# Kernel optimization log

Measured on AMD Instinct MI355X. Metric: run time of the kernel, lower is better.

## Reference

```python
import jax, jax.numpy as jnp
import numpy as np
import math

B, C, H, W = 8, 256, 64, 64
CQK = C // 8

def _conv1x1(x, w, b):
    # x: [B,C,H,W], w: [O,C], b: [O]  (1x1 conv == per-pixel linear)
    return jnp.einsum('bchw,oc->bohw', x, w) + b[None, :, None, None]

def setup_inputs() -> dict:
    key = jax.random.key(0)
    ks = jax.random.split(key, 7)
    inputs = jax.random.normal(ks[0], (B, C, H, W), dtype=jnp.float32)
    # init_weight: normal(0, sqrt(2/(k*k*out_channels))) for 1x1 convs
    wq = jax.random.normal(ks[1], (CQK, C), dtype=jnp.float32) * math.sqrt(2.0 / CQK)
    wk = jax.random.normal(ks[2], (CQK, C), dtype=jnp.float32) * math.sqrt(2.0 / CQK)
    wv = jax.random.normal(ks[3], (C, C), dtype=jnp.float32) * math.sqrt(2.0 / C)
    bq = jnp.zeros((CQK,), dtype=jnp.float32)
    bk = jnp.zeros((CQK,), dtype=jnp.float32)
    bv = jnp.zeros((C,), dtype=jnp.float32)
    # torch init is zeros(1); use nonzero so the attention path contributes
    alpha = jnp.full((1,), 0.5, dtype=jnp.float32)
    return {"inputs": inputs, "wq": wq, "bq": bq, "wk": wk, "bk": bk,
            "wv": wv, "bv": bv, "alpha": alpha}

def reference(inputs, wq, bq, wk, bk, wv, bv, alpha):
    b, c, h, w = inputs.shape
    n = h * w
    q = _conv1x1(inputs, wq, bq).reshape(b, -1, n)          # [B, C/8, N]
    k = _conv1x1(inputs, wk, bk).reshape(b, -1, n)          # [B, C/8, N]
    v = _conv1x1(inputs, wv, bv).reshape(b, c, n)           # [B, C, N]
    # attention_weight[b, i, j] = q[:, i] . k[:, j]
    attn = jnp.einsum('bdi,bdj->bij', q, k)                 # [B, N, N]
    attn = jax.nn.softmax(attn, axis=-1)
    # value @ attn^T : out[b, c, i] = sum_j v[b, c, j] * attn[b, i, j]
    out = jnp.einsum('bcj,bij->bci', v, attn)               # [B, C, N]
    return alpha[0] * out.reshape(inputs.shape) + inputs
```

## Files before the change

### kernel.cpp

```cpp
#include <hip/hip_runtime.h>
#include <math.h>

#define B_  8
#define C_  256
#define N_  4096
#define NJC (N_ / 128)
#define PLD 136

using frag  = __attribute__((ext_vector_type(8))) short;
using f32x4 = __attribute__((ext_vector_type(4))) float;

__device__ __forceinline__ unsigned short f2bf(float f) {
    unsigned u = __float_as_uint(f);
    u += 0x7fffu + ((u >> 16) & 1u);
    return (unsigned short)(u >> 16);
}
__device__ __forceinline__ float bf2f(unsigned short h) {
    return __uint_as_float(((unsigned)h) << 16);
}
#define PK2(a, b) (((unsigned)(a)) | (((unsigned)(b)) << 16))

__device__ __forceinline__ f32x4 fmax4(f32x4 a, f32x4 b) {
    f32x4 r;
    r[0] = fmaxf(a[0], b[0]); r[1] = fmaxf(a[1], b[1]);
    r[2] = fmaxf(a[2], b[2]); r[3] = fmaxf(a[3], b[3]);
    return r;
}

__global__ __launch_bounds__(256) void wprep_kernel(
    const float* __restrict__ wq, const float* __restrict__ wk,
    const float* __restrict__ wv,
    unsigned short* __restrict__ whf, unsigned short* __restrict__ wlf)
{
    const int fid  = blockIdx.x * 256 + threadIdx.x;
    if (fid >= 20 * 8 * 64) return;
    const int g    = fid >> 9;
    const int kc   = (fid >> 6) & 7;
    const int lane = fid & 63;
    const int r16  = lane & 15, q = lane >> 4;

    const float* src; int row;
    if (g < 2)      { src = wq; row = g * 16 + r16; }
    else if (g < 4) { src = wk; row = (g - 2) * 16 + r16; }
    else            { src = wv; row = (g - 4) * 16 + r16; }

    const float* wp = src + row * 256 + kc * 32 + q * 8;
    float v[8];
#pragma unroll
    for (int j = 0; j < 8; ++j) v[j] = wp[j];

    unsigned short h[8];
#pragma unroll
    for (int j = 0; j < 8; ++j) h[j] = f2bf(v[j]);
    uint4 U;
    U.x = PK2(h[0], h[1]); U.y = PK2(h[2], h[3]);
    U.z = PK2(h[4], h[5]); U.w = PK2(h[6], h[7]);
    *(uint4*)&whf[(size_t)fid * 8] = U;

    if (g < 4) {
        unsigned short l[8];
#pragma unroll
        for (int j = 0; j < 8; ++j) l[j] = f2bf(v[j] - bf2f(h[j]));
        uint4 V;
        V.x = PK2(l[0], l[1]); V.y = PK2(l[2], l[3]);
        V.z = PK2(l[4], l[5]); V.w = PK2(l[6], l[7]);
        *(uint4*)&wlf[(size_t)fid * 8] = V;
    }
}

__global__ __launch_bounds__(256, 2) void proj_kernel(
    const float* __restrict__ x,
    const float* __restrict__ bq, const float* __restrict__ bk,
    const float* __restrict__ bv,
    const unsigned short* __restrict__ whf, const unsigned short* __restrict__ wlf,
    unsigned short* __restrict__ qh, unsigned short* __restrict__ ql,
    unsigned short* __restrict__ kh, unsigned short* __restrict__ kl,
    unsigned short* __restrict__ vbf)
{
    __shared__ unsigned xpk[64 * 260 + 4];

    const int tid  = threadIdx.x;
    const int w    = tid >> 6;
    const int lane = tid & 63;
    const int quad = lane >> 4;
    const int l16  = lane & 15;
    const int n0   = blockIdx.x * 64;
    const int b    = blockIdx.y;

    {
        const int p  = tid & 63;
        const int cb = tid >> 6;
        const float* xbase = x + (size_t)b * C_ * N_ + n0 + p;
#pragma unroll 16
        for (int s = 0; s < 64; ++s) {
            const int c = s * 4 + cb;
            const float v = xbase[(size_t)c * N_];
            const unsigned short hb = f2bf(v);
            const unsigned short lb = f2bf(v - bf2f(hb));
            xpk[p * 260 + c] = (((unsigned)hb) << 16) | lb;
        }
    }
    __syncthreads();

    const frag* wh = (const frag*)whf;
    const frag* wl = (const frag*)wlf;
    const int n = n0 + w * 16 + l16;

    f32x4 acc[20];
#pragma unroll
    for (int g = 0; g < 20; ++g) acc[g] = (f32x4){0.f, 0.f, 0.f, 0.f};

    for (int kc = 0; kc < 8; ++kc) {
        const unsigned* row = &xpk[(w * 16 + l16) * 260 + kc * 32 + quad * 8];
        const uint4 A  = *(const uint4*)row;
        const uint4 Bv = *(const uint4*)(row + 4);
        frag bh, bl;
        unsigned* bhp = (unsigned*)&bh;
        unsigned* blp = (unsigned*)&bl;
        bhp[0] = __builtin_amdgcn_perm(A.y,  A.x,  0x07060302u);
        bhp[1] = __builtin_amdgcn_perm(A.w,  A.z,  0x07060302u);
        bhp[2] = __builtin_amdgcn_perm(Bv.y, Bv.x, 0x07060302u);
        bhp[3] = __builtin_amdgcn_perm(Bv.w, Bv.z, 0x07060302u);
        blp[0] = __builtin_amdgcn_perm(A.y,  A.x,  0x05040100u);
        blp[1] = __builtin_amdgcn_perm(A.w,  A.z,  0x05040100u);
        blp[2] = __builtin_amdgcn_perm(Bv.y, Bv.x, 0x05040100u);
        blp[3] = __builtin_amdgcn_perm(Bv.w, Bv.z, 0x05040100u);

#pragma unroll
        for (int g = 0; g < 4; ++g) {
            const frag ah = wh[(g * 8 + kc) * 64 + lane];
            const frag al = wl[(g * 8 + kc) * 64 + lane];
            acc[g] = __builtin_amdgcn_mfma_f32_16x16x32_bf16(ah, bh, acc[g], 0, 0, 0);
            acc[g] = __builtin_amdgcn_mfma_f32_16x16x32_bf16(al, bh, acc[g], 0, 0, 0);
            acc[g] = __builtin_amdgcn_mfma_f32_16x16x32_bf16(ah, bl, acc[g], 0, 0, 0);
        }
#pragma unroll
        for (int g = 4; g < 20; ++g) {
            const frag ah = wh[(g * 8 + kc) * 64 + lane];
            acc[g] = __builtin_amdgcn_mfma_f32_16x16x32_bf16(ah, bh, acc[g], 0, 0, 0);
        }
    }

#pragma unroll
    for (int g = 0; g < 4; ++g) {
        const bool isq = (g < 2);
        const float* bias = isq ? bq : bk;
        const int dbase = (isq ? g : g - 2) * 16 + quad * 4;
        unsigned short hs[4], ls[4];
#pragma unroll
        for (int r = 0; r < 4; ++r) {
            const float f = acc[g][r] + bias[dbase + r];
            hs[r] = f2bf(f);
            ls[r] = f2bf(f - bf2f(hs[r]));
        }
        const size_t off = ((size_t)(b * N_ + n)) * 32 + dbase;
        *(uint2*)&(isq ? qh : kh)[off] = make_uint2(PK2(hs[0], hs[1]), PK2(hs[2], hs[3]));
        *(uint2*)&(isq ? ql : kl)[off] = make_uint2(PK2(ls[0], ls[1]), PK2(ls[2], ls[3]));
    }
#pragma unroll
    for (int g = 4; g < 20; ++g) {
#pragma unroll
        for (int r = 0; r < 4; ++r) {
            const int c = (g - 4) * 16 + quad * 4 + r;
            vbf[((size_t)b * C_ + c) * N_ + n] = f2bf(acc[g][r] + bv[c]);
        }
    }
}

__global__ __launch_bounds__(512, 2) void attn_kernel(
    const unsigned short* __restrict__ qh, const unsigned short* __restrict__ ql,
    const unsigned short* __restrict__ khg, const unsigned short* __restrict__ klg,
    const unsigned short* __restrict__ vbf,
    const float* __restrict__ x, const float* __restrict__ alpha_p,
    float* __restrict__ out)
{
    __shared__ __align__(16) short kbuf[2][2][128 * 32];
    __shared__ __align__(16) short p_s[2][128 * PLD];
    __shared__ float alpha_s[2][128];
    __shared__ float l_s[128];

    const int tid  = threadIdx.x;
    const int w    = tid >> 6;
    const int lane = tid & 63;
    const int quad = lane >> 4;
    const int l16  = lane & 15;
    const int b    = blockIdx.y;
    const int i0   = blockIdx.x * 128;

    const size_t qoff = ((size_t)(b * N_ + i0 + w * 16 + l16)) * 32 + quad * 8;
    const frag qhf = *(const frag*)(qh + qoff);
    const frag qlf = *(const frag*)(ql + qoff);

    const unsigned short* khb = khg + (size_t)b * N_ * 32;
    const unsigned short* klb = klg + (size_t)b * N_ * 32;
    const unsigned short* vb  = vbf + (size_t)b * C_ * N_;

    f32x4 o[8][2];
#pragma unroll
    for (int it = 0; it < 8; ++it) {
        o[it][0] = (f32x4){0.f, 0.f, 0.f, 0.f};
        o[it][1] = (f32x4){0.f, 0.f, 0.f, 0.f};
    }

    float m_run = -INFINITY, l_run = 0.f;

    const int stoff = w * 512 + lane * 8;

    {
        const uint4 h0 = *(const uint4*)(khb + stoff);
        const uint4 l0 = *(const uint4*)(klb + stoff);
        *(uint4*)&kbuf[0][0][stoff] = h0;
        *(uint4*)&kbuf[0][1][stoff] = l0;
    }
    __syncthreads();

    for (int jc = 0; jc < NJC; ++jc) {
        const int bf = jc & 1;

        f32x4 st[8];
#pragma unroll
        for (int js = 0; js < 8; ++js) {
            const frag ka = *(const frag*)&kbuf[bf][0][(js * 16 + l16) * 32 + quad * 8];
            const frag kb2 = *(const frag*)&kbuf[bf][1][(js * 16 + l16) * 32 + quad * 8];
            f32x4 s = (f32x4){0.f, 0.f, 0.f, 0.f};
            s = __builtin_amdgcn_mfma_f32_16x16x32_bf16(ka, qhf, s, 0, 0, 0);
            s = __builtin_amdgcn_mfma_f32_16x16x32_bf16(ka, qlf, s, 0, 0, 0);
            s = __builtin_amdgcn_mfma_f32_16x16x32_bf16(kb2, qhf, s, 0, 0, 0);
            st[js] = s;
        }

        const int jn = (jc + 1 < NJC) ? jc + 1 : jc;
        const uint4 knh = *(const uint4*)(khb + (size_t)jn * 4096 + stoff);
        const uint4 knl = *(const uint4*)(klb + (size_t)jn * 4096 + stoff);

        f32x4 t0 = fmax4(fmax4(st[0], st[1]), fmax4(st[2], st[3]));
        f32x4 t1 = fmax4(fmax4(st[4], st[5]), fmax4(st[6], st[7]));
        t0 = fmax4(t0, t1);
        float mx = fmaxf(fmaxf(t0[0], t0[1]), fmaxf(t0[2], t0[3]));
        mx = fmaxf(mx, __shfl_xor(mx, 16));
        mx = fmaxf(mx, __shfl_xor(mx, 32));
        const float mnew = fmaxf(m_run, mx);
        const float sc   = __expf(m_run - mnew);

        f32x4 ps4 = (f32x4){0.f, 0.f, 0.f, 0.f};
#pragma unroll
        for (int js = 0; js < 8; ++js) {
#pragma unroll
            for (int r = 0; r < 4; ++r) st[js][r] = __expf(st[js][r] - mnew);
            ps4[0] += st[js][0]; ps4[1] += st[js][1];
            ps4[2] += st[js][2]; ps4[3] += st[js][3];
        }
        float ps = (ps4[0] + ps4[1]) + (ps4[2] + ps4[3]);
        ps += __shfl_xor(ps, 16);
        ps += __shfl_xor(ps, 32);
        l_run = l_run * sc + ps;
        m_run = mnew;
        if (quad == 0) alpha_s[bf][w * 16 + l16] = sc;

#pragma unroll
        for (int js = 0; js < 8; ++js) {
            const unsigned a0 = __float_as_uint(st[js][0]) + 0x8000u;
            const unsigned a1 = __float_as_uint(st[js][1]) + 0x8000u;
            const unsigned a2 = __float_as_uint(st[js][2]) + 0x8000u;
            const unsigned a3 = __float_as_uint(st[js][3]) + 0x8000u;
            const unsigned p01 = __builtin_amdgcn_perm(a1, a0, 0x07060302u);
            const unsigned p23 = __builtin_amdgcn_perm(a3, a2, 0x07060302u);
            *(uint2*)&p_s[bf][(w * 16 + l16) * PLD + js * 16 + quad * 4] =
                make_uint2(p01, p23);
        }

        *(uint4*)&kbuf[bf ^ 1][0][stoff] = knh;
        *(uint4*)&kbuf[bf ^ 1][1][stoff] = knl;

        __syncthreads();

        frag vf[4][2];
#pragma unroll
        for (int ks = 0; ks < 4; ++ks)
#pragma unroll
            for (int ct = 0; ct < 2; ++ct)
                vf[ks][ct] = *(const frag*)(vb
                    + (size_t)(w * 32 + ct * 16 + l16) * N_
                    + jc * 128 + ks * 32 + quad * 8);

#pragma unroll
        for (int it = 0; it < 8; ++it)
#pragma unroll
            for (int r = 0; r < 4; ++r) {
                const float al = alpha_s[bf][it * 16 + quad * 4 + r];
                o[it][0][r] *= al;
                o[it][1][r] *= al;
            }

#pragma unroll
        for (int ks = 0; ks < 4; ++ks) {
#pragma unroll
            for (int it = 0; it < 8; ++it) {
                const frag pf = *(const frag*)&p_s[bf][(it * 16 + l16) * PLD
                                                       + ks * 32 + quad * 8];
                o[it][0] = __builtin_amdgcn_mfma_f32_16x16x32_bf16(pf, vf[ks][0], o[it][0], 0, 0, 0);
                o[it][1] = __builtin_amdgcn_mfma_f32_16x16x32_bf16(pf, vf[ks][1], o[it][1], 0, 0, 0);
            }
        }
    }

    if (quad == 0) l_s[w * 16 + l16] = l_run;
    __syncthreads();
    const float av = alpha_p[0];

#pragma unroll
    for (int it = 0; it < 8; ++it) {
        float invl[4];
#pragma unroll
        for (int r = 0; r < 4; ++r) invl[r] = 1.f / l_s[it * 16 + quad * 4 + r];
#pragma unroll
        for (int ct = 0; ct < 2; ++ct) {
            const int c = w * 32 + ct * 16 + l16;
            const size_t base = (size_t)b * C_ * N_ + (size_t)c * N_
                                + i0 + it * 16 + quad * 4;
            const float4 xv = *(const float4*)(x + base);
            float4 ov;
            ov.x = av * (o[it][ct][0] * invl[0]) + xv.x;
            ov.y = av * (o[it][ct][1] * invl[1]) + xv.y;
            ov.z = av * (o[it][ct][2] * invl[2]) + xv.z;
            ov.w = av * (o[it][ct][3] * invl[3]) + xv.w;
            *(float4*)(out + base) = ov;
        }
    }
}

extern "C" void kernel_launch(void* const* d_in, const int* in_sizes, int n_in,
                              void* d_out, int out_size, void* d_ws, size_t ws_size,
                              hipStream_t stream)
{
    const float* x  = (const float*)d_in[0];
    const float* wq = (const float*)d_in[1];
    const float* bq = (const float*)d_in[2];
    const float* wk = (const float*)d_in[3];
    const float* bk = (const float*)d_in[4];
    const float* wv = (const float*)d_in[5];
    const float* bv = (const float*)d_in[6];
    const float* al = (const float*)d_in[7];
    float* out = (float*)d_out;

    char* ws = (char*)d_ws;
    unsigned short* qh  = (unsigned short*)(ws + 0);
    unsigned short* ql  = (unsigned short*)(ws + (size_t)2  * 1024 * 1024);
    unsigned short* kh  = (unsigned short*)(ws + (size_t)4  * 1024 * 1024);
    unsigned short* kl  = (unsigned short*)(ws + (size_t)6  * 1024 * 1024);
    unsigned short* vbf = (unsigned short*)(ws + (size_t)8  * 1024 * 1024);
    unsigned short* whf = (unsigned short*)(ws + (size_t)24 * 1024 * 1024);
    unsigned short* wlf = (unsigned short*)(ws + (size_t)24 * 1024 * 1024 + 256 * 1024);

    wprep_kernel<<<40, 256, 0, stream>>>(wq, wk, wv, whf, wlf);
    proj_kernel<<<dim3(N_ / 64, B_), 256, 0, stream>>>(
        x, bq, bk, bv, whf, wlf, qh, ql, kh, kl, vbf);
    attn_kernel<<<dim3(N_ / 128, B_), 512, 0, stream>>>(
        qh, ql, kh, kl, vbf, x, al, out);
}
```

Before: 232.4 us.

## Use fragment-ordered LDS layouts for K and P; load x directly into registers in projection

After: 238.2 us. +2.5%, slower.

```diff
diff --git a/kernel.cpp b/kernel.cpp
--- a/kernel.cpp
+++ b/kernel.cpp
@@ -5,7 +5,6 @@
 #define C_  256
 #define N_  4096
 #define NJC (N_ / 128)
-#define PLD 136
 
 using frag  = __attribute__((ext_vector_type(8))) short;
 using f32x4 = __attribute__((ext_vector_type(4))) float;
@@ -77,8 +76,6 @@
     unsigned short* __restrict__ kh, unsigned short* __restrict__ kl,
     unsigned short* __restrict__ vbf)
 {
-    __shared__ unsigned xpk[64 * 260 + 4];
-
     const int tid  = threadIdx.x;
     const int w    = tid >> 6;
     const int lane = tid & 63;
@@ -86,45 +83,35 @@
     const int l16  = lane & 15;
     const int n0   = blockIdx.x * 64;
     const int b    = blockIdx.y;
-
+    const int n    = n0 + w * 16 + l16;
+
+    float xr[64];
     {
-        const int p  = tid & 63;
-        const int cb = tid >> 6;
-        const float* xbase = x + (size_t)b * C_ * N_ + n0 + p;
-#pragma unroll 16
-        for (int s = 0; s < 64; ++s) {
-            const int c = s * 4 + cb;
-            const float v = xbase[(size_t)c * N_];
-            const unsigned short hb = f2bf(v);
-            const unsigned short lb = f2bf(v - bf2f(hb));
-            xpk[p * 260 + c] = (((unsigned)hb) << 16) | lb;
-        }
-    }
-    __syncthreads();
+        const float* xp = x + (size_t)b * C_ * N_ + (size_t)(quad * 8) * N_ + n;
+#pragma unroll
+        for (int kc = 0; kc < 8; ++kc)
+#pragma unroll
+            for (int j = 0; j < 8; ++j)
+                xr[kc * 8 + j] = xp[(size_t)(kc * 32 + j) * N_];
+    }
 
     const frag* wh = (const frag*)whf;
     const frag* wl = (const frag*)wlf;
-    const int n = n0 + w * 16 + l16;
 
     f32x4 acc[20];
 #pragma unroll
     for (int g = 0; g < 20; ++g) acc[g] = (f32x4){0.f, 0.f, 0.f, 0.f};
 
+#pragma unroll
     for (int kc = 0; kc < 8; ++kc) {
-        const unsigned* row = &xpk[(w * 16 + l16) * 260 + kc * 32 + quad * 8];
-        const uint4 A  = *(const uint4*)row;
-        const uint4 Bv = *(const uint4*)(row + 4);
         frag bh, bl;
-        unsigned* bhp = (unsigned*)&bh;
-        unsigned* blp = (unsigned*)&bl;
-        bhp[0] = __builtin_amdgcn_perm(A.y,  A.x,  0x07060302u);
-        bhp[1] = __builtin_amdgcn_perm(A.w,  A.z,  0x07060302u);
-        bhp[2] = __builtin_amdgcn_perm(Bv.y, Bv.x, 0x07060302u);
-        bhp[3] = __builtin_amdgcn_perm(Bv.w, Bv.z, 0x07060302u);
-        blp[0] = __builtin_amdgcn_perm(A.y,  A.x,  0x05040100u);
-        blp[1] = __builtin_amdgcn_perm(A.w,  A.z,  0x05040100u);
-        blp[2] = __builtin_amdgcn_perm(Bv.y, Bv.x, 0x05040100u);
-        blp[3] = __builtin_amdgcn_perm(Bv.w, Bv.z, 0x05040100u);
+#pragma unroll
+        for (int j = 0; j < 8; ++j) {
+            const float v = xr[kc * 8 + j];
+            const unsigned short hb = f2bf(v);
+            bh[j] = (short)hb;
+            bl[j] = (short)f2bf(v - bf2f(hb));
+        }
 
 #pragma unroll
         for (int g = 0; g < 4; ++g) {
@@ -137,7 +124,7 @@
 #pragma unroll
         for (int g = 4; g < 20; ++g) {
             const frag ah = wh[(g * 8 + kc) * 64 + lane];
-            acc[g] = __builtin_amdgcn_mfma_f32_16x16x32_bf16(ah, bh, acc[g], 0, 0, 0);
+            acc[g] = __builtin_amdgcn_mfma_f32_16x16x32_bf16(bh, ah, acc[g], 0, 0, 0);
         }
     }
 
@@ -157,13 +144,16 @@
         *(uint2*)&(isq ? qh : kh)[off] = make_uint2(PK2(hs[0], hs[1]), PK2(hs[2], hs[3]));
         *(uint2*)&(isq ? ql : kl)[off] = make_uint2(PK2(ls[0], ls[1]), PK2(ls[2], ls[3]));
     }
+
 #pragma unroll
     for (int g = 4; g < 20; ++g) {
-#pragma unroll
-        for (int r = 0; r < 4; ++r) {
-            const int c = (g - 4) * 16 + quad * 4 + r;
-            vbf[((size_t)b * C_ + c) * N_ + n] = f2bf(acc[g][r] + bv[c]);
-        }
+        const int c = (g - 4) * 16 + l16;
+        const float bb = bv[c];
+        unsigned short vs[4];
+#pragma unroll
+        for (int r = 0; r < 4; ++r) vs[r] = f2bf(acc[g][r] + bb);
+        const size_t off = ((size_t)b * C_ + c) * N_ + n0 + w * 16 + quad * 4;
+        *(uint2*)&vbf[off] = make_uint2(PK2(vs[0], vs[1]), PK2(vs[2], vs[3]));
     }
 }
 
@@ -174,8 +164,8 @@
     const float* __restrict__ x, const float* __restrict__ alpha_p,
     float* __restrict__ out)
 {
-    __shared__ __align__(16) short kbuf[2][2][128 * 32];
-    __shared__ __align__(16) short p_s[2][128 * PLD];
+    __shared__ __align__(16) short kbuf[2][2][4096];
+    __shared__ __align__(16) short p_s[2][16384];
     __shared__ float alpha_s[2][128];
     __shared__ float l_s[128];
 
@@ -187,6 +177,9 @@
     const int b    = blockIdx.y;
     const int i0   = blockIdx.x * 128;
 
+    const int knb = (tid >> 6) * 16 + (tid & 15);
+    const int kdg = ((tid >> 4) & 3) * 8;
+
     const size_t qoff = ((size_t)(b * N_ + i0 + w * 16 + l16)) * 32 + quad * 8;
     const frag qhf = *(const frag*)(qh + qoff);
     const frag qlf = *(const frag*)(ql + qoff);
@@ -204,13 +197,11 @@
 
     float m_run = -INFINITY, l_run = 0.f;
 
-    const int stoff = w * 512 + lane * 8;
-
     {
-        const uint4 h0 = *(const uint4*)(khb + stoff);
-        const uint4 l0 = *(const uint4*)(klb + stoff);
-        *(uint4*)&kbuf[0][0][stoff] = h0;
-        *(uint4*)&kbuf[0][1][stoff] = l0;
+        const uint4 h0 = *(const uint4*)(khb + (size_t)knb * 32 + kdg);
+        const uint4 l0 = *(const uint4*)(klb + (size_t)knb * 32 + kdg);
+        *(uint4*)&kbuf[0][0][tid * 8] = h0;
+        *(uint4*)&kbuf[0][1][tid * 8] = l0;
     }
     __syncthreads();
 
@@ -220,8 +211,8 @@
         f32x4 st[8];
 #pragma unroll
         for (int js = 0; js < 8; ++js) {
-            const frag ka = *(const frag*)&kbuf[bf][0][(js * 16 + l16) * 32 + quad * 8];
-            const frag kb2 = *(const frag*)&kbuf[bf][1][(js * 16 + l16) * 32 + quad * 8];
+            const frag ka  = *(const frag*)&kbuf[bf][0][(js * 64 + lane) * 8];
+            const frag kb2 = *(const frag*)&kbuf[bf][1][(js * 64 + lane) * 8];
             f32x4 s = (f32x4){0.f, 0.f, 0.f, 0.f};
             s = __builtin_amdgcn_mfma_f32_16x16x32_bf16(ka, qhf, s, 0, 0, 0);
             s = __builtin_amdgcn_mfma_f32_16x16x32_bf16(ka, qlf, s, 0, 0, 0);
@@ -230,8 +221,8 @@
         }
 
         const int jn = (jc + 1 < NJC) ? jc + 1 : jc;
-        const uint4 knh = *(const uint4*)(khb + (size_t)jn * 4096 + stoff);
-        const uint4 knl = *(const uint4*)(klb + (size_t)jn * 4096 + stoff);
+        const uint4 knh = *(const uint4*)(khb + (size_t)(jn * 128 + knb) * 32 + kdg);
+        const uint4 knl = *(const uint4*)(klb + (size_t)(jn * 128 + knb) * 32 + kdg);
 
         f32x4 t0 = fmax4(fmax4(st[0], st[1]), fmax4(st[2], st[3]));
         f32x4 t1 = fmax4(fmax4(st[4], st[5]), fmax4(st[6], st[7]));
@@ -265,12 +256,13 @@
             const unsigned a3 = __float_as_uint(st[js][3]) + 0x8000u;
             const unsigned p01 = __builtin_amdgcn_perm(a1, a0, 0x07060302u);
             const unsigned p23 = __builtin_amdgcn_perm(a3, a2, 0x07060302u);
-            *(uint2*)&p_s[bf][(w * 16 + l16) * PLD + js * 16 + quad * 4] =
+            const int F = (w * 4 + (js >> 1)) * 4 + (js & 1) * 2 + (quad >> 1);
+            *(uint2*)&p_s[bf][F * 128 + l16 * 8 + (quad & 1) * 4] =
                 make_uint2(p01, p23);
         }
 
-        *(uint4*)&kbuf[bf ^ 1][0][stoff] = knh;
-        *(uint4*)&kbuf[bf ^ 1][1][stoff] = knl;
+        *(uint4*)&kbuf[bf ^ 1][0][tid * 8] = knh;
+        *(uint4*)&kbuf[bf ^ 1][1][tid * 8] = knl;
 
         __syncthreads();
 
@@ -296,8 +288,8 @@
         for (int ks = 0; ks < 4; ++ks) {
 #pragma unroll
             for (int it = 0; it < 8; ++it) {
-                const frag pf = *(const frag*)&p_s[bf][(it * 16 + l16) * PLD
-                                                       + ks * 32 + quad * 8];
+                const int F = (it * 4 + ks) * 4 + quad;
+                const frag pf = *(const frag*)&p_s[bf][F * 128 + l16 * 8];
                 o[it][0] = __builtin_amdgcn_mfma_f32_16x16x32_bf16(pf, vf[ks][0], o[it][0], 0, 0, 0);
                 o[it][1] = __builtin_amdgcn_mfma_f32_16x16x32_bf16(pf, vf[ks][1], o[it][1], 0, 0, 0);
             }
```
